# Optimization experiments

Measured on AMD Instinct MI355X. Metric: run time of the kernel, lower is better.

The kernel has to match this reference:

```python
import jax, jax.numpy as jnp
import numpy as np

B, T, D, H, L = 4, 2048, 256, 4, 2
HD = D // H
VOCAB, MAX_BITS, MLP_H = 32, 64, 64


def setup_inputs() -> dict:
    key = jax.random.key(0)
    ks = jax.random.split(key, 20)
    s = 0.02
    n = lambda k, shp: (jax.random.normal(k, shp, jnp.float32) * s)
    inp = {
        'tokens': jax.random.randint(ks[0], (B, T), 0, VOCAB),
        'embed': n(ks[1], (VOCAB, D)),
        'ln1_w': jnp.ones((L, D)), 'ln1_b': jnp.zeros((L, D)),
        'qkv_w': n(ks[2], (L, D, 3 * D)), 'qkv_b': jnp.zeros((L, 3 * D)),
        'proj_w': n(ks[3], (L, D, D)), 'proj_b': jnp.zeros((L, D)),
        'ln2_w': jnp.ones((L, D)), 'ln2_b': jnp.zeros((L, D)),
        'ffn1_w': n(ks[4], (L, D, 4 * D)), 'ffn1_b': jnp.zeros((L, 4 * D)),
        'ffn2_w': n(ks[5], (L, 4 * D, D)), 'ffn2_b': jnp.zeros((L, D)),
        'lnf_w': jnp.ones((D,)), 'lnf_b': jnp.zeros((D,)),
        'out_queries': n(ks[6], (MAX_BITS * 2, D)),
        'outp_w': n(ks[7], (D, 1)), 'outp_b': jnp.zeros((1,)),
        'mlp_w1': n(ks[8], (3, MLP_H)), 'mlp_b1': jnp.zeros((MLP_H,)),
        'mlp_w2': n(ks[9], (MLP_H, MLP_H)), 'mlp_b2': jnp.zeros((MLP_H,)),
        'mlp_w3': n(ks[10], (MLP_H, 2)), 'mlp_b3': jnp.zeros((2,)),
    }
    return inp


def _layernorm(x, w, b, eps=1e-5):
    mu = jnp.mean(x, axis=-1, keepdims=True)
    var = jnp.mean(jnp.square(x - mu), axis=-1, keepdims=True)
    return (x - mu) * jax.lax.rsqrt(var + eps) * w + b


def _rope_tables(t_len, hd):
    inv_freq = 1.0 / (10000.0 ** (jnp.arange(0, hd, 2, dtype=jnp.float32) / hd))
    freqs = jnp.outer(jnp.arange(t_len, dtype=jnp.float32), inv_freq)  # [T, hd/2]
    emb = jnp.concatenate([freqs, freqs], axis=-1)                     # [T, hd]
    return jnp.cos(emb)[None, :, None, :], jnp.sin(emb)[None, :, None, :]


def _rotate_half(x):
    x1, x2 = x[..., : x.shape[-1] // 2], x[..., x.shape[-1] // 2:]
    return jnp.concatenate([-x2, x1], axis=-1)


def _attention(x, qkv_w, qkv_b, proj_w, proj_b):
    b, t, c = x.shape
    qkv = (x @ qkv_w + qkv_b).reshape(b, t, 3, H, HD)
    q, k, v = qkv[:, :, 0], qkv[:, :, 1], qkv[:, :, 2]  # [B,T,H,HD]
    cos, sin = _rope_tables(t, HD)
    q = q * cos + _rotate_half(q) * sin
    k = k * cos + _rotate_half(k) * sin
    scores = jnp.einsum('bthd,bshd->bhts', q, k) / jnp.sqrt(jnp.float32(HD))
    causal = jnp.tril(jnp.ones((t, t), dtype=bool))
    scores = jnp.where(causal, scores, -jnp.inf)
    attn = jax.nn.softmax(scores, axis=-1)
    out = jnp.einsum('bhts,bshd->bthd', attn, v).reshape(b, t, c)
    return out @ proj_w + proj_b


def reference(tokens, embed, ln1_w, ln1_b, qkv_w, qkv_b, proj_w, proj_b,
              ln2_w, ln2_b, ffn1_w, ffn1_b, ffn2_w, ffn2_b, lnf_w, lnf_b,
              out_queries, outp_w, outp_b,
              mlp_w1, mlp_b1, mlp_w2, mlp_b2, mlp_w3, mlp_b3):
    x = embed[tokens]  # [B,T,D]
    for l in range(L):
        x = x + _attention(_layernorm(x, ln1_w[l], ln1_b[l]),
                           qkv_w[l], qkv_b[l], proj_w[l], proj_b[l])
        h = _layernorm(x, ln2_w[l], ln2_b[l])
        h = jax.nn.gelu(h @ ffn1_w[l] + ffn1_b[l], approximate=False)
        x = x + (h @ ffn2_w[l] + ffn2_b[l])
    x = _layernorm(x, lnf_w, lnf_b)
    # query cross-attention for bit-pair selection
    q_scores = jnp.einsum('qd,btd->bqt', out_queries, x) / jnp.sqrt(jnp.float32(D))
    q_attn = jax.nn.softmax(q_scores, axis=-1)           # [B, 2*MAX_BITS, T]
    selected = jnp.einsum('bqt,btd->bqd', q_attn, x)
    bits = jax.nn.sigmoid((selected @ outp_w + outp_b)[..., 0])
    pairs = bits.reshape(-1, MAX_BITS, 2)                # [B, MAX_BITS, 2]

    # sequential full-adder over bits
    def step(carry, ab):  # carry [B], ab [B,2]
        z = jnp.concatenate([ab, carry[:, None]], axis=-1)  # [B,3]
        h = jax.nn.relu(z @ mlp_w1 + mlp_b1)
        h = jax.nn.relu(h @ mlp_w2 + mlp_b2)
        o = jax.nn.sigmoid(h @ mlp_w3 + mlp_b3)
        return o[:, 1], o[:, 0]

    carry0 = jnp.zeros((pairs.shape[0],), jnp.float32)
    carry, sum_bits = jax.lax.scan(step, carry0, jnp.swapaxes(pairs, 0, 1))
    sum_all = jnp.concatenate([sum_bits.T, carry[:, None]], axis=1)  # [B, MAX_BITS+1]
    return sum_all, pairs, q_attn
```

## Files before the change

### kernel.cpp

```cpp
#include <hip/hip_runtime.h>
#include <hip/hip_bf16.h>

#define BB 4
#define TT 2048
#define DD 256
#define HH 4
#define HDD 64
#define NROW 8192
#define NQ 128

typedef __hip_bfloat16 bf16;
typedef __attribute__((ext_vector_type(8))) short bf8v;
typedef __attribute__((ext_vector_type(4))) short bf4v;
typedef __attribute__((ext_vector_type(4))) float f4v;
typedef __attribute__((ext_vector_type(2))) unsigned int u2v;

__device__ __forceinline__ bf16 f2b(float v){ return __float2bfloat16(v); }
__device__ __forceinline__ short f2bs(float v){
    bf16 h = __float2bfloat16(v);
    return *reinterpret_cast<short*>(&h);
}
__device__ __forceinline__ float bs2f(short s){
    bf16 h = *reinterpret_cast<bf16*>(&s);
    return __bfloat162float(h);
}
__device__ __forceinline__ float rl(float v, int l){
    return __uint_as_float(__builtin_amdgcn_readlane(__float_as_uint(v), l));
}

#define DPP_ROR_ADD(v, ctrl) \
    ((v) + __int_as_float(__builtin_amdgcn_update_dpp(0, __float_as_int(v), (ctrl), 0xF, 0xF, false)))
#define DPP_ROR_MAX(v, ctrl) \
    fmaxf((v), __int_as_float(__builtin_amdgcn_update_dpp(0, __float_as_int(v), (ctrl), 0xF, 0xF, false)))

__device__ __forceinline__ void plswap16(float v, float& a, float& b){
#if __has_builtin(__builtin_amdgcn_permlane16_swap)
    u2v r = __builtin_amdgcn_permlane16_swap(__float_as_uint(v), __float_as_uint(v), false, false);
    a = __uint_as_float(r.x); b = __uint_as_float(r.y);
#else
    a = v; b = v;
    asm volatile("" : "+v"(b));
    asm("v_permlane16_swap_b32 %0, %1" : "+v"(a), "+v"(b));
#endif
}
__device__ __forceinline__ void plswap32(float v, float& a, float& b){
#if __has_builtin(__builtin_amdgcn_permlane32_swap)
    u2v r = __builtin_amdgcn_permlane32_swap(__float_as_uint(v), __float_as_uint(v), false, false);
    a = __uint_as_float(r.x); b = __uint_as_float(r.y);
#else
    a = v; b = v;
    asm volatile("" : "+v"(b));
    asm("v_permlane32_swap_b32 %0, %1" : "+v"(a), "+v"(b));
#endif
}
__device__ __forceinline__ float swap16_add(float v){ float a,b; plswap16(v,a,b); return a + b; }
__device__ __forceinline__ float swap32_add(float v){ float a,b; plswap32(v,a,b); return a + b; }
__device__ __forceinline__ float swap16_max(float v){ float a,b; plswap16(v,a,b); return fmaxf(a,b); }
__device__ __forceinline__ float swap32_max(float v){ float a,b; plswap32(v,a,b); return fmaxf(a,b); }
__device__ __forceinline__ float wsum(float v){
    v = DPP_ROR_ADD(v, 0x121); v = DPP_ROR_ADD(v, 0x122);
    v = DPP_ROR_ADD(v, 0x124); v = DPP_ROR_ADD(v, 0x128);
    v = swap16_add(v); v = swap32_add(v);
    return v;
}
__device__ __forceinline__ float wmax(float v){
    v = DPP_ROR_MAX(v, 0x121); v = DPP_ROR_MAX(v, 0x122);
    v = DPP_ROR_MAX(v, 0x124); v = DPP_ROR_MAX(v, 0x128);
    v = swap16_max(v); v = swap32_max(v);
    return v;
}

#define MFMA32(A,B,C) __builtin_amdgcn_mfma_f32_16x16x32_bf16((A),(B),(C),0,0,0)
#if __has_builtin(__builtin_amdgcn_mfma_f32_16x16x16bf16_1k)
#define MFMA16(A,B,C) __builtin_amdgcn_mfma_f32_16x16x16bf16_1k((A),(B),(C),0,0,0)
#else
__device__ __forceinline__ f4v mfma16_asm(bf4v a, bf4v b, f4v c){
    f4v d;
    asm("v_mfma_f32_16x16x16_bf16 %0, %1, %2, %3" : "=v"(d) : "v"(a), "v"(b), "v"(c));
    return d;
}
#define MFMA16(A,B,C) mfma16_asm((A),(B),(C))
#endif

__global__ __launch_bounds__(256) void k_embln(const int* __restrict__ tok,
                                               const float* __restrict__ emb,
                                               const float* __restrict__ w,
                                               const float* __restrict__ b,
                                               float* __restrict__ x,
                                               bf16* __restrict__ Y){
    int row = blockIdx.x*4 + (threadIdx.x >> 6);
    int lane = threadIdx.x & 63;
    f4v v = *(const f4v*)(emb + (long)tok[row]*DD + lane*4);
    *(f4v*)(x + (long)row*DD + lane*4) = v;
    float s  = (v[0]+v[1]) + (v[2]+v[3]);
    float s2 = (v[0]*v[0]+v[1]*v[1]) + (v[2]*v[2]+v[3]*v[3]);
    s = wsum(s); s2 = wsum(s2);
    float mu  = s * (1.0f/DD);
    float var = s2 * (1.0f/DD) - mu*mu;
    float rs  = rsqrtf(var + 1e-5f);
    f4v wv4 = *(const f4v*)(w + lane*4);
    f4v bv4 = *(const f4v*)(b + lane*4);
    bf4v o;
    #pragma unroll
    for (int i=0;i<4;i++) o[i] = f2bs((v[i]-mu)*rs*wv4[i] + bv4[i]);
    *(bf4v*)(Y + (long)row*DD + lane*4) = o;
}

__global__ __launch_bounds__(256) void k_misc(const float* __restrict__ oq, bf16* __restrict__ oqb,
                                              float* __restrict__ cosT, float* __restrict__ sinT,
                                              const float* __restrict__ w2, float* __restrict__ w2t){
    int gid = blockIdx.x*256 + threadIdx.x;
    {
        int t = gid >> 5, dd = gid & 31;
        float invf = powf(10000.0f, -(float)(2*dd)/64.0f);
        float ang = (float)t * invf;
        float sn, cs;
        sincosf(ang, &sn, &cs);
        cosT[gid] = cs; sinT[gid] = sn;
    }
    if (gid < NQ*DD) oqb[gid] = f2b(oq[gid]);
    if (gid < 4096){ int j = gid >> 6, k = gid & 63; w2t[gid] = w2[k*64 + j]; }
}

__global__ __launch_bounds__(256) void k_wtall(const float* __restrict__ qkvw,
                                               const float* __restrict__ projw,
                                               const float* __restrict__ f1w,
                                               const float* __restrict__ f2w,
                                               bf16* __restrict__ wt){
    __shared__ float t[32][33];
    int z = blockIdx.z;
    int l = z >> 2, type = z & 3;
    long L = (long)l*786432;
    int K, M; const float* src; long doff;
    if (type == 0){ K=256;  M=768;  src = qkvw + (long)l*256*768;  doff = L; }
    else if (type == 1){ K=256;  M=256;  src = projw + (long)l*256*256; doff = L + 196608; }
    else if (type == 2){ K=256;  M=1024; src = f1w  + (long)l*256*1024; doff = L + 262144; }
    else               { K=1024; M=256;  src = f2w  + (long)l*1024*256; doff = L + 524288; }
    int m0 = blockIdx.x*32, k0 = blockIdx.y*32;
    if (m0 >= M || k0 >= K) return;
    bf16* dst = wt + doff;
    int tx = threadIdx.x, ty = threadIdx.y;
    #pragma unroll
    for (int i=0;i<4;i++)
        t[ty+i*8][tx] = src[(long)(k0+ty+i*8)*M + m0 + tx];
    __syncthreads();
    #pragma unroll
    for (int i=0;i<4;i++)
        dst[(long)(m0+ty+i*8)*K + k0 + tx] = f2b(t[tx][ty+i*8]);
}

__global__ __launch_bounds__(256) void k_lnb(const float* __restrict__ X,
                                             const float* __restrict__ w,
                                             const float* __restrict__ b,
                                             bf16* __restrict__ Y){
    int row = blockIdx.x*4 + (threadIdx.x >> 6);
    int lane = threadIdx.x & 63;
    f4v v = *(const f4v*)(X + (long)row*DD + lane*4);
    float s  = (v[0]+v[1]) + (v[2]+v[3]);
    float s2 = (v[0]*v[0]+v[1]*v[1]) + (v[2]*v[2]+v[3]*v[3]);
    s = wsum(s); s2 = wsum(s2);
    float mu  = s * (1.0f/DD);
    float var = s2 * (1.0f/DD) - mu*mu;
    float rs  = rsqrtf(var + 1e-5f);
    f4v wv4 = *(const f4v*)(w + lane*4);
    f4v bv4 = *(const f4v*)(b + lane*4);
    bf4v o;
    #pragma unroll
    for (int i=0;i<4;i++) o[i] = f2bs((v[i]-mu)*rs*wv4[i] + bv4[i]);
    *(bf4v*)(Y + (long)row*DD + lane*4) = o;
}

__global__ __launch_bounds__(256) void k_lnf(const float* __restrict__ X,
                                             const float* __restrict__ w,
                                             const float* __restrict__ b,
                                             const float* __restrict__ ow,
                                             bf16* __restrict__ Yb,
                                             float* __restrict__ g){
    int row = blockIdx.x*4 + (threadIdx.x >> 6);
    int lane = threadIdx.x & 63;
    f4v v = *(const f4v*)(X + (long)row*DD + lane*4);
    float s  = (v[0]+v[1]) + (v[2]+v[3]);
    float s2 = (v[0]*v[0]+v[1]*v[1]) + (v[2]*v[2]+v[3]*v[3]);
    s = wsum(s); s2 = wsum(s2);
    float mu  = s * (1.0f/DD);
    float var = s2 * (1.0f/DD) - mu*mu;
    float rs  = rsqrtf(var + 1e-5f);
    f4v wv4 = *(const f4v*)(w + lane*4);
    f4v bv4 = *(const f4v*)(b + lane*4);
    f4v ov4 = *(const f4v*)(ow + lane*4);
    bf4v o;
    float gp = 0.f;
    #pragma unroll
    for (int i=0;i<4;i++){
        float y = (v[i]-mu)*rs*wv4[i] + bv4[i];
        o[i] = f2bs(y);
        gp += y * ov4[i];
    }
    *(bf4v*)(Yb + (long)row*DD + lane*4) = o;
    gp = wsum(gp);
    if (lane == 0) g[row] = gp;
}

__global__ __launch_bounds__(256) void k_mgemm(const bf16* __restrict__ A,
                                               const bf16* __restrict__ Wt,
                                               const float* __restrict__ bias,
                                               float* __restrict__ Cf,
                                               bf16* __restrict__ Cb,
                                               int K, int M, int mode){
    __shared__ short As[128*32];
    __shared__ short Ws[64*32];
    int tid = threadIdx.x;
    int lane = tid & 63, wv = tid >> 6;
    int n0 = blockIdx.y * 128, m0 = blockIdx.x * 64;
    int rbase = (wv >> 1) * 64, cbase = (wv & 1) * 32;
    f4v acc[4][2] = {};
    int s2 = tid + 256;
    for (int k0 = 0; k0 < K; k0 += 32){
        bf8v va0 = *(const bf8v*)(A  + (long)(n0 + (tid>>2))*K + k0 + ((tid&3)<<3));
        bf8v va1 = *(const bf8v*)(A  + (long)(n0 + (s2 >>2))*K + k0 + ((s2 &3)<<3));
        bf8v vw  = *(const bf8v*)(Wt + (long)(m0 + (tid>>2))*K + k0 + ((tid&3)<<3));
        __syncthreads();
        *(bf8v*)&As[tid*8] = va0;
        *(bf8v*)&As[s2 *8] = va1;
        *(bf8v*)&Ws[tid*8] = vw;
        __syncthreads();
        bf8v af[4], bfr[2];
        int k8 = (lane >> 4) << 3;
        #pragma unroll
        for (int i=0;i<4;i++) af[i]  = *(bf8v*)&As[(rbase + i*16 + (lane&15))*32 + k8];
        #pragma unroll
        for (int j=0;j<2;j++) bfr[j] = *(bf8v*)&Ws[(cbase + j*16 + (lane&15))*32 + k8];
        #pragma unroll
        for (int i=0;i<4;i++)
            #pragma unroll
            for (int j=0;j<2;j++)
                acc[i][j] = MFMA32(af[i], bfr[j], acc[i][j]);
    }
    int rq = (lane >> 4) * 4;
    int cl = lane & 15;
    #pragma unroll
    for (int i=0;i<4;i++){
        #pragma unroll
        for (int j=0;j<2;j++){
            int m = m0 + cbase + j*16 + cl;
            float bs = bias[m];
            #pragma unroll
            for (int r=0;r<4;r++){
                int n = n0 + rbase + i*16 + rq + r;
                float v = acc[i][j][r] + bs;
                long idx = (long)n*M + m;
                if (mode == 0)      Cf[idx] = v;
                else if (mode == 1) Cf[idx] += v;
                else if (mode == 2) Cb[idx] = f2b(0.5f*v*(1.0f + erff(v*0.70710678118654752f)));
                else                Cb[idx] = f2b(v);
            }
        }
    }
}

__global__ __launch_bounds__(256) void k_mgemmQKV(const bf16* __restrict__ A,
                                                  const bf16* __restrict__ Wt,
                                                  const float* __restrict__ bias,
                                                  const float* __restrict__ cosT,
                                                  const float* __restrict__ sinT,
                                                  bf16* __restrict__ qb,
                                                  bf16* __restrict__ kb,
                                                  bf16* __restrict__ vt){
    __shared__ short As[128*32];
    __shared__ short Ws[64*32];
    __shared__ short E[128][68];
    const int K = 256, M = 768;
    int tid = threadIdx.x;
    int lane = tid & 63, wv = tid >> 6;
    int n0 = blockIdx.y * 128, m0 = blockIdx.x * 64;
    int rbase = (wv >> 1) * 64, cbase = (wv & 1) * 32;
    f4v acc[4][2] = {};
    int s2 = tid + 256;
    for (int k0 = 0; k0 < K; k0 += 32){
        bf8v va0 = *(const bf8v*)(A  + (long)(n0 + (tid>>2))*K + k0 + ((tid&3)<<3));
        bf8v va1 = *(const bf8v*)(A  + (long)(n0 + (s2 >>2))*K + k0 + ((s2 &3)<<3));
        bf8v vw  = *(const bf8v*)(Wt + (long)(m0 + (tid>>2))*K + k0 + ((tid&3)<<3));
        __syncthreads();
        *(bf8v*)&As[tid*8] = va0;
        *(bf8v*)&As[s2 *8] = va1;
        *(bf8v*)&Ws[tid*8] = vw;
        __syncthreads();
        bf8v af[4], bfr[2];
        int k8 = (lane >> 4) << 3;
        #pragma unroll
        for (int i=0;i<4;i++) af[i]  = *(bf8v*)&As[(rbase + i*16 + (lane&15))*32 + k8];
        #pragma unroll
        for (int j=0;j<2;j++) bfr[j] = *(bf8v*)&Ws[(cbase + j*16 + (lane&15))*32 + k8];
        #pragma unroll
        for (int i=0;i<4;i++)
            #pragma unroll
            for (int j=0;j<2;j++)
                acc[i][j] = MFMA32(af[i], bfr[j], acc[i][j]);
    }
    int rq = (lane >> 4) * 4;
    int cl = lane & 15;
    #pragma unroll
    for (int i=0;i<4;i++){
        #pragma unroll
        for (int j=0;j<2;j++){
            int cc = cbase + j*16 + cl;
            float bs = bias[m0 + cc];
            #pragma unroll
            for (int r=0;r<4;r++)
                E[rbase + i*16 + rq + r][cc] = f2bs(acc[i][j][r] + bs);
        }
    }
    __syncthreads();
    int part = m0 >> 8;
    int h = (m0 >> 6) & 3;
    int b = n0 >> 11;
    int t0 = n0 & 2047;
    int bh = b*HH + h;
    if (part < 2){
        bf16* dst0 = part ? kb : qb;
        int r2 = tid >> 2;
        int c0 = (tid & 3) * 16;
        int cpx = c0 ^ 32;
        #pragma unroll
        for (int half=0; half<2; half++){
            int row = half*64 + r2;
            int t = t0 + row;
            bf8v e0 = *(bf8v*)&E[row][c0];
            bf8v e1 = *(bf8v*)&E[row][c0+8];
            bf8v p0 = *(bf8v*)&E[row][cpx];
            bf8v p1 = *(bf8v*)&E[row][cpx+8];
            const float* ct = cosT + t*32;
            const float* st = sinT + t*32;
            short o[16];
            #pragma unroll
            for (int i=0;i<8;i++){
                int d = c0 + i, dd = d & 31;
                float cs = ct[dd], sn = st[dd];
                float v = bs2f(e0[i]), v2 = bs2f(p0[i]);
                o[i] = f2bs((d < 32) ? (v*cs - v2*sn) : (v*cs + v2*sn));
            }
            #pragma unroll
            for (int i=0;i<8;i++){
                int d = c0 + 8 + i, dd = d & 31;
                float cs = ct[dd], sn = st[dd];
                float v = bs2f(e1[i]), v2 = bs2f(p1[i]);
                o[8+i] = f2bs((d < 32) ? (v*cs - v2*sn) : (v*cs + v2*sn));
            }
            short* dp = (short*)dst0 + ((long)bh*TT + t)*64 + c0;
            *(bf8v*)dp     = *(bf8v*)&o[0];
            *(bf8v*)(dp+8) = *(bf8v*)&o[8];
        }
    } else {
        int tIdx0 = t0 >> 6;
        int d  = (tid & 127) >> 1;
        int k0 = (tid & 1) * 32;
        int tt = tid >> 7;
        short o[32];
        #pragma unroll
        for (int k=0;k<32;k++) o[k] = E[tt*64 + k0 + k][d];
        short* dp = (short*)vt + (((long)bh*32 + tIdx0 + tt)*64 + d)*64 + k0;
        *(bf8v*)dp      = *(bf8v*)&o[0];
        *(bf8v*)(dp+8)  = *(bf8v*)&o[8];
        *(bf8v*)(dp+16) = *(bf8v*)&o[16];
        *(bf8v*)(dp+24) = *(bf8v*)&o[24];
    }
}

__global__ __launch_bounds__(256) void k_fattn(const bf16* __restrict__ qb,
                                               const bf16* __restrict__ kb,
                                               const bf16* __restrict__ vt,
                                               bf16* __restrict__ ob){
    __shared__ short Ks[2][64][72];
    __shared__ short Vs[2][64][68];
    int bh = blockIdx.y;
    int qt = (int)(gridDim.x - 1) - (int)blockIdx.x;
    int tid = threadIdx.x;
    int lane = tid & 63, w = tid >> 6;
    int col = lane & 15, quad = lane >> 4;
    int q0 = qt*64 + w*16;
    const bf16* qp = qb + ((long)bh*TT + q0 + col)*64 + quad*8;
    bf8v bq0 = *(const bf8v*)(qp);
    bf8v bq1 = *(const bf8v*)(qp + 32);
    f4v oc[4] = {};
    float lsum = 0.f;
    int qglob = q0 + col;
    int srow = tid >> 2, sc0 = (tid & 3) * 16;
    const short* kgb = (const short*)kb + ((long)bh*TT + srow)*64 + sc0;
    const short* vgb = (const short*)vt + (((long)bh*32)*64 + srow)*64 + sc0;

    bf8v pk0 = *(const bf8v*)kgb;
    bf8v pk1 = *(const bf8v*)(kgb + 8);
    bf8v pv0 = *(const bf8v*)vgb;
    bf8v pv1 = *(const bf8v*)(vgb + 8);
    *(bf8v*)&Ks[0][srow][sc0]     = pk0;
    *(bf8v*)&Ks[0][srow][sc0 + 8] = pk1;
    *(bf8v*)&Vs[0][srow][sc0]     = pv0;
    *(bf8v*)&Vs[0][srow][sc0 + 8] = pv1;

    int buf = 0;
    for (int kt=0; kt<=qt; kt++){
        __syncthreads();
        bool more = (kt < qt);
        if (more){
            const short* kg = kgb + (long)(kt+1)*4096;
            const short* vg = vgb + (long)(kt+1)*4096;
            pk0 = *(const bf8v*)kg;
            pk1 = *(const bf8v*)(kg + 8);
            pv0 = *(const bf8v*)vg;
            pv1 = *(const bf8v*)(vg + 8);
        }
        bool diag = (kt == qt);
        int ntmax = diag ? w : 3;
        bf4v bp[4];
        #pragma unroll
        for (int nt=0; nt<4; nt++){
            if (nt > ntmax) continue;
            bf8v ka0 = *(const bf8v*)&Ks[buf][nt*16 + col][quad*8];
            bf8v ka1 = *(const bf8v*)&Ks[buf][nt*16 + col][32 + quad*8];
            f4v st = {};
            st = MFMA32(ka0, bq0, st);
            st = MFMA32(ka1, bq1, st);
            int key0 = kt*64 + nt*16 + quad*4;
            bf4v pb;
            #pragma unroll
            for (int r=0; r<4; r++){
                float e = __expf(st[r]*0.125f);
                if (diag && (key0 + r > qglob)) e = 0.f;
                lsum += e;
                pb[r] = f2bs(e);
            }
            bp[nt] = pb;
        }
        #pragma unroll
        for (int dt=0; dt<4; dt++){
            #pragma unroll
            for (int nt=0; nt<4; nt++){
                if (nt > ntmax) continue;
                bf4v va = *(const bf4v*)&Vs[buf][dt*16 + col][nt*16 + quad*4];
                oc[dt] = MFMA16(va, bp[nt], oc[dt]);
            }
        }
        if (more){
            *(bf8v*)&Ks[buf^1][srow][sc0]     = pk0;
            *(bf8v*)&Ks[buf^1][srow][sc0 + 8] = pk1;
            *(bf8v*)&Vs[buf^1][srow][sc0]     = pv0;
            *(bf8v*)&Vs[buf^1][srow][sc0 + 8] = pv1;
        }
        buf ^= 1;
    }
    lsum += __shfl_xor(lsum, 16, 64);
    lsum += __shfl_xor(lsum, 32, 64);
    float linv = 1.0f / lsum;

    int b = bh / HH, h = bh % HH;
    long obase = ((long)b*TT + q0 + col)*DD + h*64 + quad*4;
    #pragma unroll
    for (int dt=0; dt<4; dt++){
        bf4v o4;
        #pragma unroll
        for (int r=0; r<4; r++) o4[r] = f2bs(oc[dt][r]*linv);
        *(bf4v*)(ob + obase + dt*16) = o4;
    }
}

__global__ __launch_bounds__(256) void k_score(const bf16* __restrict__ oqb,
                                               const bf16* __restrict__ xfb,
                                               float* __restrict__ S){
    int b = blockIdx.y, t0 = blockIdx.x*64;
    int tid = threadIdx.x, lane = tid & 63, w = tid >> 6;
    int col = lane & 15, quad = lane >> 4, k8 = quad << 3;
    const bf16* xb = xfb + (long)b*TT*DD;
    f4v acc[2][4] = {};
    #pragma unroll
    for (int ko=0; ko<8; ko++){
        int kk = ko*32 + k8;
        bf8v a0 = *(const bf8v*)(oqb + (long)(w*32 +      col)*DD + kk);
        bf8v a1 = *(const bf8v*)(oqb + (long)(w*32 + 16 + col)*DD + kk);
        #pragma unroll
        for (int bt=0; bt<4; bt++){
            bf8v bv = *(const bf8v*)(xb + (long)(t0 + bt*16 + col)*DD + kk);
            acc[0][bt] = MFMA32(a0, bv, acc[0][bt]);
            acc[1][bt] = MFMA32(a1, bv, acc[1][bt]);
        }
    }
    #pragma unroll
    for (int qt2=0; qt2<2; qt2++){
        #pragma unroll
        for (int bt=0; bt<4; bt++){
            #pragma unroll
            for (int r=0; r<4; r++){
                int q = w*32 + qt2*16 + quad*4 + r;
                S[((long)b*NQ + q)*TT + t0 + bt*16 + col] = acc[qt2][bt][r]*0.0625f;
            }
        }
    }
}

__global__ __launch_bounds__(256) void k_psoft(const float* __restrict__ S,
                                               const float* __restrict__ g,
                                               const float* __restrict__ obias,
                                               float* __restrict__ out_qattn,
                                               float* __restrict__ out_pairs,
                                               float* __restrict__ bits){
    __shared__ float cmax[4], cs[4], cg[4];
    int bq = blockIdx.x, b = bq >> 7;
    int tid = threadIdx.x, wv = tid >> 6, lane = tid & 63;
    const f4v* S4 = (const f4v*)(S + (long)bq*TT);
    f4v s0 = S4[tid], s1 = S4[tid + 256];
    float lmax = fmaxf(fmaxf(fmaxf(s0[0],s0[1]), fmaxf(s0[2],s0[3])),
                       fmaxf(fmaxf(s1[0],s1[1]), fmaxf(s1[2],s1[3])));
    lmax = wmax(lmax);
    if (lane == 0) cmax[wv] = lmax;
    __syncthreads();
    float m = fmaxf(fmaxf(cmax[0],cmax[1]), fmaxf(cmax[2],cmax[3]));
    const f4v* g4 = (const f4v*)(g + (long)b*TT);
    f4v gv0 = g4[tid], gv1 = g4[tid + 256];
    f4v e0, e1;
    #pragma unroll
    for (int i=0;i<4;i++){ e0[i] = __expf(s0[i]-m); e1[i] = __expf(s1[i]-m); }
    float lsum = (e0[0]+e0[1]+e0[2]+e0[3]) + (e1[0]+e1[1]+e1[2]+e1[3]);
    float gdot = (e0[0]*gv0[0]+e0[1]*gv0[1]+e0[2]*gv0[2]+e0[3]*gv0[3])
               + (e1[0]*gv1[0]+e1[1]*gv1[1]+e1[2]*gv1[2]+e1[3]*gv1[3]);
    lsum = wsum(lsum); gdot = wsum(gdot);
    if (lane == 0){ cs[wv] = lsum; cg[wv] = gdot; }
    __syncthreads();
    float Lr = (cs[0]+cs[1]) + (cs[2]+cs[3]);
    float G  = (cg[0]+cg[1]) + (cg[2]+cg[3]);
    float inv = 1.0f / Lr;
    f4v* out4 = (f4v*)(out_qattn + (long)bq*TT);
    out4[tid]       = e0 * inv;
    out4[tid + 256] = e1 * inv;
    if (tid == 0){
        float bit = 1.0f/(1.0f + expf(-(G*inv + obias[0])));
        bits[bq] = bit;
        out_pairs[bq] = bit;
    }
}

__global__ __launch_bounds__(64) void k_scan(const float* __restrict__ bits,
                                             const float* __restrict__ w1, const float* __restrict__ b1,
                                             const float* __restrict__ w2t, const float* __restrict__ b2,
                                             const float* __restrict__ w3, const float* __restrict__ b3,
                                             float* __restrict__ out_sum){
    __shared__ __align__(16) float h1s[2][64];
    int b = blockIdx.x, lane = threadIdx.x;
    float w1c0 = w1[lane], w1c1 = w1[64 + lane], w1c2 = w1[128 + lane];
    float b1v = b1[lane], b2v = b2[lane];
    float w3c0 = w3[lane*2 + 0], w3c1 = w3[lane*2 + 1];
    float b30 = b3[0], b31 = b3[1];
    const f4v* wrow = (const f4v*)(w2t + (long)lane*64);
    f4v c0v = wrow[0],  c1v = wrow[1],  c2v = wrow[2],  c3v = wrow[3],
        c4v = wrow[4],  c5v = wrow[5],  c6v = wrow[6],  c7v = wrow[7],
        c8v = wrow[8],  c9v = wrow[9],  cav = wrow[10], cbv = wrow[11],
        ccv = wrow[12], cdv = wrow[13], cev = wrow[14], cfv = wrow[15];
    float z0v = bits[b*128 + lane*2 + 0];
    float z1v = bits[b*128 + lane*2 + 1];
    float carry = 0.f;
    for (int step=0; step<64; step++){
        float z0 = rl(z0v, step);
        float z1 = rl(z1v, step);
        float h1 = fmaxf(z0*w1c0 + z1*w1c1 + carry*w1c2 + b1v, 0.f);
        float* hb = h1s[step & 1];
        hb[lane] = h1;
        __syncthreads();
        const f4v* hv = (const f4v*)hb;
        f4v va = hv[0]*c0v,  vb = hv[1]*c1v,  vc = hv[2]*c2v,   vd = hv[3]*c3v;
        va += hv[4]*c4v;   vb += hv[5]*c5v;   vc += hv[6]*c6v;   vd += hv[7]*c7v;
        va += hv[8]*c8v;   vb += hv[9]*c9v;   vc += hv[10]*cav;  vd += hv[11]*cbv;
        va += hv[12]*ccv;  vb += hv[13]*cdv;  vc += hv[14]*cev;  vd += hv[15]*cfv;
        f4v vs = (va + vb) + (vc + vd);
        float h2 = fmaxf(((vs[0] + vs[1]) + (vs[2] + vs[3])) + b2v, 0.f);
        float t0 = h2*w3c0, t1 = h2*w3c1;
        t0 = DPP_ROR_ADD(t0, 0x121); t1 = DPP_ROR_ADD(t1, 0x121);
        t0 = DPP_ROR_ADD(t0, 0x122); t1 = DPP_ROR_ADD(t1, 0x122);
        t0 = DPP_ROR_ADD(t0, 0x124); t1 = DPP_ROR_ADD(t1, 0x124);
        t0 = DPP_ROR_ADD(t0, 0x128); t1 = DPP_ROR_ADD(t1, 0x128);
        t0 = swap16_add(t0); t1 = swap16_add(t1);
        t0 = swap32_add(t0); t1 = swap32_add(t1);
        float o0 = 1.0f/(1.0f + __expf(-(t0 + b30)));
        carry    = 1.0f/(1.0f + __expf(-(t1 + b31)));
        if (lane == 0) out_sum[b*65 + step] = o0;
    }
    if (lane == 0) out_sum[b*65 + 64] = carry;
}

extern "C" void kernel_launch(void* const* d_in, const int* in_sizes, int n_in,
                              void* d_out, int out_size, void* d_ws, size_t ws_size,
                              hipStream_t stream){
    const int*   tok   = (const int*)d_in[0];
    const float* emb   = (const float*)d_in[1];
    const float* ln1w  = (const float*)d_in[2];
    const float* ln1b  = (const float*)d_in[3];
    const float* qkvw  = (const float*)d_in[4];
    const float* qkvb  = (const float*)d_in[5];
    const float* projw = (const float*)d_in[6];
    const float* projb = (const float*)d_in[7];
    const float* ln2w  = (const float*)d_in[8];
    const float* ln2b  = (const float*)d_in[9];
    const float* f1w   = (const float*)d_in[10];
    const float* f1b   = (const float*)d_in[11];
    const float* f2w   = (const float*)d_in[12];
    const float* f2bb  = (const float*)d_in[13];
    const float* lnfw  = (const float*)d_in[14];
    const float* lnfb  = (const float*)d_in[15];
    const float* oq    = (const float*)d_in[16];
    const float* ow    = (const float*)d_in[17];
    const float* obias = (const float*)d_in[18];
    const float* w1    = (const float*)d_in[19];
    const float* b1    = (const float*)d_in[20];
    const float* w2    = (const float*)d_in[21];
    const float* b2    = (const float*)d_in[22];
    const float* w3    = (const float*)d_in[23];
    const float* b3    = (const float*)d_in[24];
    float* out = (float*)d_out;

    const long MB = 1048576;
    char* W = (char*)d_ws;
    float* x     = (float*)(W);
    bf16*  attnb = (bf16*)(W + 8*MB);
    bf16*  hb    = (bf16*)(W + 16*MB);
    bf16*  qb    = (bf16*)(W + 32*MB);
    bf16*  kb    = (bf16*)(W + 36*MB);
    bf16*  vt    = (bf16*)(W + 44*MB);
    bf16*  xnb   = (bf16*)(W + 48*MB);
    bf16*  wt    = (bf16*)(W + 52*MB);
    float* bits  = (float*)(W + 55*MB);
    bf16*  oqb   = (bf16*)(W + 56*MB);
    float* cosT  = (float*)(W + 57*MB);
    float* sinT  = cosT + 65536;
    float* w2t   = (float*)(W + 58*MB);
    bf16*  xfb   = (bf16*)(W + 32*MB);
    float* g     = (float*)(W + 36*MB);
    float* S     = (float*)(W + 40*MB);

    k_wtall<<<dim3(32, 32, 8), dim3(32,8), 0, stream>>>(qkvw, projw, f1w, f2w, wt);
    k_misc<<<256, 256, 0, stream>>>(oq, oqb, cosT, sinT, w2, w2t);

    k_embln<<<NROW/4, 256, 0, stream>>>(tok, emb, ln1w, ln1b, x, xnb);
    for (int l=0; l<2; l++){
        long L = (long)l*786432;
        if (l) k_lnb<<<NROW/4, 256, 0, stream>>>(x, ln1w + l*DD, ln1b + l*DD, xnb);
        k_mgemmQKV<<<dim3(768/64, 64), 256, 0, stream>>>(
            xnb, wt + L, qkvb + l*768, cosT, sinT, qb, kb, vt);
        k_fattn<<<dim3(TT/64, BB*HH), 256, 0, stream>>>(qb, kb, vt, attnb);
        k_mgemm<<<dim3(256/64, 64), 256, 0, stream>>>(
            attnb, wt + L + 196608, projb + l*DD, x, (bf16*)0, 256, 256, 1);
        k_lnb<<<NROW/4, 256, 0, stream>>>(x, ln2w + l*DD, ln2b + l*DD, xnb);
        k_mgemm<<<dim3(1024/64, 64), 256, 0, stream>>>(
            xnb, wt + L + 262144, f1b + l*1024, (float*)0, hb, 256, 1024, 2);
        k_mgemm<<<dim3(256/64, 64), 256, 0, stream>>>(
            hb, wt + L + 524288, f2bb + l*DD, x, (bf16*)0, 1024, 256, 1);
    }
    k_lnf<<<NROW/4, 256, 0, stream>>>(x, lnfw, lnfb, ow, xfb, g);
    k_score<<<dim3(TT/64, BB), 256, 0, stream>>>(oqb, xfb, S);
    k_psoft<<<BB*NQ, 256, 0, stream>>>(S, g, obias, out + 772, out + 260, bits);
    k_scan<<<4, 64, 0, stream>>>(bits, w1, b1, w2t, b2, w3, b3, out);
}
```

Measured before the change: 397.7 us.

## Use direct global-to-LDS loads in GEMMs and halve attention query tile

The two GEMM kernels now copy their A and W tiles with global_load_lds instead of loading into registers and storing to shared memory, which cuts register traffic and VALU work in the staging step. The flash-attention kernel drops to 32-query blocks of 128 threads. Each thread stages twice as much K/V per tile, and the causal diagonal mask is adjusted for odd and even half-tiles. This doubles the grid and the attention parallelism, but K/V reuse per block falls, and the LDS layout written by the direct loads must match what the MFMA fragment reads expect.

```diff
diff --git a/kernel.cpp b/kernel.cpp
--- a/kernel.cpp
+++ b/kernel.cpp
@@ -26,6 +26,11 @@
 }
 __device__ __forceinline__ float rl(float v, int l){
     return __uint_as_float(__builtin_amdgcn_readlane(__float_as_uint(v), l));
+}
+
+__device__ __forceinline__ void gll16(const void* g, void* l){
+    __builtin_amdgcn_global_load_lds((const __attribute__((address_space(1))) unsigned int*)g,
+                                     (__attribute__((address_space(3))) unsigned int*)l, 16, 0, 0);
 }
 
 #define DPP_ROR_ADD(v, ctrl) \
@@ -215,14 +220,12 @@
     int rbase = (wv >> 1) * 64, cbase = (wv & 1) * 32;
     f4v acc[4][2] = {};
     int s2 = tid + 256;
+    int wvo = wv * 512;
     for (int k0 = 0; k0 < K; k0 += 32){
-        bf8v va0 = *(const bf8v*)(A  + (long)(n0 + (tid>>2))*K + k0 + ((tid&3)<<3));
-        bf8v va1 = *(const bf8v*)(A  + (long)(n0 + (s2 >>2))*K + k0 + ((s2 &3)<<3));
-        bf8v vw  = *(const bf8v*)(Wt + (long)(m0 + (tid>>2))*K + k0 + ((tid&3)<<3));
         __syncthreads();
-        *(bf8v*)&As[tid*8] = va0;
-        *(bf8v*)&As[s2 *8] = va1;
-        *(bf8v*)&Ws[tid*8] = vw;
+        gll16(A  + (long)(n0 + (tid>>2))*K + k0 + ((tid&3)<<3), &As[wvo]);
+        gll16(A  + (long)(n0 + (s2 >>2))*K + k0 + ((s2 &3)<<3), &As[2048 + wvo]);
+        gll16(Wt + (long)(m0 + (tid>>2))*K + k0 + ((tid&3)<<3), &Ws[wvo]);
         __syncthreads();
         bf8v af[4], bfr[2];
         int k8 = (lane >> 4) << 3;
@@ -276,14 +279,12 @@
     int rbase = (wv >> 1) * 64, cbase = (wv & 1) * 32;
     f4v acc[4][2] = {};
     int s2 = tid + 256;
+    int wvo = wv * 512;
     for (int k0 = 0; k0 < K; k0 += 32){
-        bf8v va0 = *(const bf8v*)(A  + (long)(n0 + (tid>>2))*K + k0 + ((tid&3)<<3));
-        bf8v va1 = *(const bf8v*)(A  + (long)(n0 + (s2 >>2))*K + k0 + ((s2 &3)<<3));
-        bf8v vw  = *(const bf8v*)(Wt + (long)(m0 + (tid>>2))*K + k0 + ((tid&3)<<3));
         __syncthreads();
-        *(bf8v*)&As[tid*8] = va0;
-        *(bf8v*)&As[s2 *8] = va1;
-        *(bf8v*)&Ws[tid*8] = vw;
+        gll16(A  + (long)(n0 + (tid>>2))*K + k0 + ((tid&3)<<3), &As[wvo]);
+        gll16(A  + (long)(n0 + (s2 >>2))*K + k0 + ((s2 &3)<<3), &As[2048 + wvo]);
+        gll16(Wt + (long)(m0 + (tid>>2))*K + k0 + ((tid&3)<<3), &Ws[wvo]);
         __syncthreads();
         bf8v af[4], bfr[2];
         int k8 = (lane >> 4) << 3;
@@ -366,7 +367,7 @@
     }
 }
 
-__global__ __launch_bounds__(256) void k_fattn(const bf16* __restrict__ qb,
+__global__ __launch_bounds__(128) void k_fattn(const bf16* __restrict__ qb,
                                                const bf16* __restrict__ kb,
                                                const bf16* __restrict__ vt,
                                                bf16* __restrict__ ob){
@@ -377,40 +378,49 @@
     int tid = threadIdx.x;
     int lane = tid & 63, w = tid >> 6;
     int col = lane & 15, quad = lane >> 4;
-    int q0 = qt*64 + w*16;
+    int q0 = qt*32 + w*16;
     const bf16* qp = qb + ((long)bh*TT + q0 + col)*64 + quad*8;
     bf8v bq0 = *(const bf8v*)(qp);
     bf8v bq1 = *(const bf8v*)(qp + 32);
     f4v oc[4] = {};
     float lsum = 0.f;
     int qglob = q0 + col;
-    int srow = tid >> 2, sc0 = (tid & 3) * 16;
+    int ktmax = qt >> 1;
+    int srow = tid >> 1, sc0 = (tid & 1) * 32;
     const short* kgb = (const short*)kb + ((long)bh*TT + srow)*64 + sc0;
     const short* vgb = (const short*)vt + (((long)bh*32)*64 + srow)*64 + sc0;
 
-    bf8v pk0 = *(const bf8v*)kgb;
+    bf8v pk0 = *(const bf8v*)(kgb);
     bf8v pk1 = *(const bf8v*)(kgb + 8);
-    bf8v pv0 = *(const bf8v*)vgb;
+    bf8v pk2 = *(const bf8v*)(kgb + 16);
+    bf8v pk3 = *(const bf8v*)(kgb + 24);
+    bf8v pv0 = *(const bf8v*)(vgb);
     bf8v pv1 = *(const bf8v*)(vgb + 8);
-    *(bf8v*)&Ks[0][srow][sc0]     = pk0;
-    *(bf8v*)&Ks[0][srow][sc0 + 8] = pk1;
-    *(bf8v*)&Vs[0][srow][sc0]     = pv0;
-    *(bf8v*)&Vs[0][srow][sc0 + 8] = pv1;
+    bf8v pv2 = *(const bf8v*)(vgb + 16);
+    bf8v pv3 = *(const bf8v*)(vgb + 24);
+    *(bf8v*)&Ks[0][srow][sc0]      = pk0;
+    *(bf8v*)&Ks[0][srow][sc0 + 8]  = pk1;
+    *(bf8v*)&Ks[0][srow][sc0 + 16] = pk2;
+    *(bf8v*)&Ks[0][srow][sc0 + 24] = pk3;
+    *(bf8v*)&Vs[0][srow][sc0]      = pv0;
+    *(bf8v*)&Vs[0][srow][sc0 + 8]  = pv1;
+    *(bf8v*)&Vs[0][srow][sc0 + 16] = pv2;
+    *(bf8v*)&Vs[0][srow][sc0 + 24] = pv3;
 
     int buf = 0;
-    for (int kt=0; kt<=qt; kt++){
+    for (int kt=0; kt<=ktmax; kt++){
         __syncthreads();
-        bool more = (kt < qt);
+        bool more = (kt < ktmax);
         if (more){
             const short* kg = kgb + (long)(kt+1)*4096;
             const short* vg = vgb + (long)(kt+1)*4096;
-            pk0 = *(const bf8v*)kg;
-            pk1 = *(const bf8v*)(kg + 8);
-            pv0 = *(const bf8v*)vg;
-            pv1 = *(const bf8v*)(vg + 8);
-        }
-        bool diag = (kt == qt);
-        int ntmax = diag ? w : 3;
+            pk0 = *(const bf8v*)(kg);      pk1 = *(const bf8v*)(kg + 8);
+            pk2 = *(const bf8v*)(kg + 16); pk3 = *(const bf8v*)(kg + 24);
+            pv0 = *(const bf8v*)(vg);      pv1 = *(const bf8v*)(vg + 8);
+            pv2 = *(const bf8v*)(vg + 16); pv3 = *(const bf8v*)(vg + 24);
+        }
+        bool diag = (kt == ktmax);
+        int ntmax = diag ? ((qt & 1) ? 2 + w : w) : 3;
         bf4v bp[4];
         #pragma unroll
         for (int nt=0; nt<4; nt++){
@@ -441,10 +451,14 @@
             }
         }
         if (more){
-            *(bf8v*)&Ks[buf^1][srow][sc0]     = pk0;
-            *(bf8v*)&Ks[buf^1][srow][sc0 + 8] = pk1;
-            *(bf8v*)&Vs[buf^1][srow][sc0]     = pv0;
-            *(bf8v*)&Vs[buf^1][srow][sc0 + 8] = pv1;
+            *(bf8v*)&Ks[buf^1][srow][sc0]      = pk0;
+            *(bf8v*)&Ks[buf^1][srow][sc0 + 8]  = pk1;
+            *(bf8v*)&Ks[buf^1][srow][sc0 + 16] = pk2;
+            *(bf8v*)&Ks[buf^1][srow][sc0 + 24] = pk3;
+            *(bf8v*)&Vs[buf^1][srow][sc0]      = pv0;
+            *(bf8v*)&Vs[buf^1][srow][sc0 + 8]  = pv1;
+            *(bf8v*)&Vs[buf^1][srow][sc0 + 16] = pv2;
+            *(bf8v*)&Vs[buf^1][srow][sc0 + 24] = pv3;
         }
         buf ^= 1;
     }
@@ -642,7 +656,7 @@
         if (l) k_lnb<<<NROW/4, 256, 0, stream>>>(x, ln1w + l*DD, ln1b + l*DD, xnb);
         k_mgemmQKV<<<dim3(768/64, 64), 256, 0, stream>>>(
             xnb, wt + L, qkvb + l*768, cosT, sinT, qb, kb, vt);
-        k_fattn<<<dim3(TT/64, BB*HH), 256, 0, stream>>>(qb, kb, vt, attnb);
+        k_fattn<<<dim3(TT/32, BB*HH), 128, 0, stream>>>(qb, kb, vt, attnb);
         k_mgemm<<<dim3(256/64, 64), 256, 0, stream>>>(
             attnb, wt + L + 196608, projb + l*DD, x, (bf16*)0, 256, 256, 1);
         k_lnb<<<NROW/4, 256, 0, stream>>>(x, ln2w + l*DD, ln2b + l*DD, xnb);
```

New measurement: 403.9 us. No clear change (+1.6%).

## Use direct global-to-LDS loads in GEMMs and drop LDS staging in attention

Applied to the files above, without the earlier changes.

The two GEMM kernels now stage A and W tiles with global_load_lds (direct global-to-LDS DMA), which avoids the round trip through registers. The flash attention kernel no longer double-buffers K and V tiles through shared memory. Each wave instead reads its K and V fragments straight from global memory, relying on L1/L2 caching, and the per-tile __syncthreads barriers go away. In exchange, attention issues more, smaller global loads with no software prefetch, and its latency now rests on cache hits.

```diff
diff --git a/kernel.cpp b/kernel.cpp
--- a/kernel.cpp
+++ b/kernel.cpp
@@ -26,6 +26,11 @@
 }
 __device__ __forceinline__ float rl(float v, int l){
     return __uint_as_float(__builtin_amdgcn_readlane(__float_as_uint(v), l));
+}
+
+__device__ __forceinline__ void gll16(const void* g, void* l){
+    __builtin_amdgcn_global_load_lds((const __attribute__((address_space(1))) unsigned int*)g,
+                                     (__attribute__((address_space(3))) unsigned int*)l, 16, 0, 0);
 }
 
 #define DPP_ROR_ADD(v, ctrl) \
@@ -215,14 +220,12 @@
     int rbase = (wv >> 1) * 64, cbase = (wv & 1) * 32;
     f4v acc[4][2] = {};
     int s2 = tid + 256;
+    int wvo = wv * 512;
     for (int k0 = 0; k0 < K; k0 += 32){
-        bf8v va0 = *(const bf8v*)(A  + (long)(n0 + (tid>>2))*K + k0 + ((tid&3)<<3));
-        bf8v va1 = *(const bf8v*)(A  + (long)(n0 + (s2 >>2))*K + k0 + ((s2 &3)<<3));
-        bf8v vw  = *(const bf8v*)(Wt + (long)(m0 + (tid>>2))*K + k0 + ((tid&3)<<3));
         __syncthreads();
-        *(bf8v*)&As[tid*8] = va0;
-        *(bf8v*)&As[s2 *8] = va1;
-        *(bf8v*)&Ws[tid*8] = vw;
+        gll16(A  + (long)(n0 + (tid>>2))*K + k0 + ((tid&3)<<3), &As[wvo]);
+        gll16(A  + (long)(n0 + (s2 >>2))*K + k0 + ((s2 &3)<<3), &As[2048 + wvo]);
+        gll16(Wt + (long)(m0 + (tid>>2))*K + k0 + ((tid&3)<<3), &Ws[wvo]);
         __syncthreads();
         bf8v af[4], bfr[2];
         int k8 = (lane >> 4) << 3;
@@ -276,14 +279,12 @@
     int rbase = (wv >> 1) * 64, cbase = (wv & 1) * 32;
     f4v acc[4][2] = {};
     int s2 = tid + 256;
+    int wvo = wv * 512;
     for (int k0 = 0; k0 < K; k0 += 32){
-        bf8v va0 = *(const bf8v*)(A  + (long)(n0 + (tid>>2))*K + k0 + ((tid&3)<<3));
-        bf8v va1 = *(const bf8v*)(A  + (long)(n0 + (s2 >>2))*K + k0 + ((s2 &3)<<3));
-        bf8v vw  = *(const bf8v*)(Wt + (long)(m0 + (tid>>2))*K + k0 + ((tid&3)<<3));
         __syncthreads();
-        *(bf8v*)&As[tid*8] = va0;
-        *(bf8v*)&As[s2 *8] = va1;
-        *(bf8v*)&Ws[tid*8] = vw;
+        gll16(A  + (long)(n0 + (tid>>2))*K + k0 + ((tid&3)<<3), &As[wvo]);
+        gll16(A  + (long)(n0 + (s2 >>2))*K + k0 + ((s2 &3)<<3), &As[2048 + wvo]);
+        gll16(Wt + (long)(m0 + (tid>>2))*K + k0 + ((tid&3)<<3), &Ws[wvo]);
         __syncthreads();
         bf8v af[4], bfr[2];
         int k8 = (lane >> 4) << 3;
@@ -370,8 +371,6 @@
                                                const bf16* __restrict__ kb,
                                                const bf16* __restrict__ vt,
                                                bf16* __restrict__ ob){
-    __shared__ short Ks[2][64][72];
-    __shared__ short Vs[2][64][68];
     int bh = blockIdx.y;
     int qt = (int)(gridDim.x - 1) - (int)blockIdx.x;
     int tid = threadIdx.x;
@@ -384,39 +383,19 @@
     f4v oc[4] = {};
     float lsum = 0.f;
     int qglob = q0 + col;
-    int srow = tid >> 2, sc0 = (tid & 3) * 16;
-    const short* kgb = (const short*)kb + ((long)bh*TT + srow)*64 + sc0;
-    const short* vgb = (const short*)vt + (((long)bh*32)*64 + srow)*64 + sc0;
-
-    bf8v pk0 = *(const bf8v*)kgb;
-    bf8v pk1 = *(const bf8v*)(kgb + 8);
-    bf8v pv0 = *(const bf8v*)vgb;
-    bf8v pv1 = *(const bf8v*)(vgb + 8);
-    *(bf8v*)&Ks[0][srow][sc0]     = pk0;
-    *(bf8v*)&Ks[0][srow][sc0 + 8] = pk1;
-    *(bf8v*)&Vs[0][srow][sc0]     = pv0;
-    *(bf8v*)&Vs[0][srow][sc0 + 8] = pv1;
-
-    int buf = 0;
+    const short* kB = (const short*)kb + ((long)bh*TT)*64;
+    const short* vB = (const short*)vt + ((long)bh*32)*4096;
+
     for (int kt=0; kt<=qt; kt++){
-        __syncthreads();
-        bool more = (kt < qt);
-        if (more){
-            const short* kg = kgb + (long)(kt+1)*4096;
-            const short* vg = vgb + (long)(kt+1)*4096;
-            pk0 = *(const bf8v*)kg;
-            pk1 = *(const bf8v*)(kg + 8);
-            pv0 = *(const bf8v*)vg;
-            pv1 = *(const bf8v*)(vg + 8);
-        }
         bool diag = (kt == qt);
         int ntmax = diag ? w : 3;
         bf4v bp[4];
         #pragma unroll
         for (int nt=0; nt<4; nt++){
             if (nt > ntmax) continue;
-            bf8v ka0 = *(const bf8v*)&Ks[buf][nt*16 + col][quad*8];
-            bf8v ka1 = *(const bf8v*)&Ks[buf][nt*16 + col][32 + quad*8];
+            const short* kr = kB + (long)(kt*64 + nt*16 + col)*64 + quad*8;
+            bf8v ka0 = *(const bf8v*)(kr);
+            bf8v ka1 = *(const bf8v*)(kr + 32);
             f4v st = {};
             st = MFMA32(ka0, bq0, st);
             st = MFMA32(ka1, bq1, st);
@@ -431,22 +410,16 @@
             }
             bp[nt] = pb;
         }
+        const short* vT = vB + (long)kt*4096;
         #pragma unroll
         for (int dt=0; dt<4; dt++){
             #pragma unroll
             for (int nt=0; nt<4; nt++){
                 if (nt > ntmax) continue;
-                bf4v va = *(const bf4v*)&Vs[buf][dt*16 + col][nt*16 + quad*4];
+                bf4v va = *(const bf4v*)(vT + (dt*16 + col)*64 + nt*16 + quad*4);
                 oc[dt] = MFMA16(va, bp[nt], oc[dt]);
             }
         }
-        if (more){
-            *(bf8v*)&Ks[buf^1][srow][sc0]     = pk0;
-            *(bf8v*)&Ks[buf^1][srow][sc0 + 8] = pk1;
-            *(bf8v*)&Vs[buf^1][srow][sc0]     = pv0;
-            *(bf8v*)&Vs[buf^1][srow][sc0 + 8] = pv1;
-        }
-        buf ^= 1;
     }
     lsum += __shfl_xor(lsum, 16, 64);
     lsum += __shfl_xor(lsum, 32, 64);
```

New measurement: 654.1 us. 64.5% more time.
